# Optimization experiments

Measured on AMD Instinct MI355X. Metric: run time of the kernel, lower is better.

Reference implementation:

```python
import jax, jax.numpy as jnp
import numpy as np

EOS = 0
INCLUDE_EOS = True
INS_COST = 1.0
DEL_COST = 1.0
SUB_COST = 1.0


def _seq_lens(tok):
    # tok: (T, N) int tokens; length = index of first EOS (+1 if included), else T
    T = tok.shape[0]
    is_eos = tok == EOS
    has = is_eos.any(axis=0)
    idx = jnp.argmax(is_eos, axis=0)
    return jnp.where(has, idx + (1 if INCLUDE_EOS else 0), T)


def _edit_distance(ref, hyp, ref_lens, hyp_lens):
    # ref: (R, N), hyp: (H, N). Levenshtein DP, scan over hyp steps.
    # The sequential deletion dependence along the ref axis is turned into a
    # min-plus prefix scan: new_row[j] = j*del + cummin_k<=j (cand[k] - k*del).
    R, N = ref.shape
    H = hyp.shape[0]
    offs = (jnp.arange(R + 1, dtype=jnp.float32) * DEL_COST)[:, None]  # (R+1,1)
    row0 = jnp.broadcast_to(offs, (R + 1, N)) + jnp.zeros((R + 1, N), jnp.float32)

    def step(row, xs):
        i, h = xs  # i: 1-based hyp step, h: (N,) hyp tokens at this step
        sub_c = SUB_COST * (ref != h[None, :]).astype(jnp.float32)  # (R,N)
        cand = jnp.concatenate(
            [row[:1] + INS_COST,
             jnp.minimum(row[1:] + INS_COST, row[:-1] + sub_c)], axis=0)
        new_row = jax.lax.cummin(cand - offs, axis=0) + offs
        # freeze rows for sequences whose hypothesis already ended
        row = jnp.where(i <= hyp_lens[None, :], new_row, row)
        return row, None

    row, _ = jax.lax.scan(step, row0, (jnp.arange(1, H + 1), hyp))
    # distance at (hyp_len, ref_len) per sequence
    return jnp.take_along_axis(row, ref_lens[None, :], axis=0)[0]


def setup_inputs() -> dict:
    key = jax.random.key(0)
    k1, k2, k3 = jax.random.split(key, 3)
    log_probs = jax.random.normal(k1, (128, 64), dtype=jnp.float32)
    ref = jax.random.randint(k2, (256, 128), 0, 1000, dtype=jnp.int64)
    hyp = jax.random.randint(k3, (256, 128, 64), 0, 1000, dtype=jnp.int64)
    return {"log_probs": log_probs, "ref": ref, "hyp": hyp}


def reference(log_probs, ref, hyp):
    batch_size, samples = log_probs.shape
    R = ref.shape[0]
    H = hyp.shape[0]
    # ref is 2D: broadcast across samples (same reference per batch element)
    ref_flat = jnp.repeat(ref[:, :, None], samples, axis=2).reshape(R, batch_size * samples)
    hyp_flat = hyp.reshape(H, batch_size * samples)
    ref_lens = _seq_lens(ref_flat)
    hyp_lens = _seq_lens(hyp_flat)
    dist = _edit_distance(ref_flat, hyp_flat, ref_lens, hyp_lens)
    er = dist / ref_lens.astype(jnp.float32)  # norm=True -> error rate
    er = er.reshape(batch_size, samples)
    er = er - er.mean(axis=1, keepdims=True)  # sub_avg=True
    loss = er * jax.nn.softmax(log_probs, axis=1)
    return loss.mean()  # reduction='mean'
```

## Files before the change

kernel.cpp:

```cpp
#include <hip/hip_runtime.h>
#include <stdint.h>


#define BATCH   128
#define SAMPLES 64
#define RLEN    256
#define HLEN    256
#define NSEQ    (BATCH*SAMPLES)
#define NTOK    1000
#define NWW     8
#define SPB     32
#define PMSTR   9
#define HTSTR   36

typedef unsigned long long u64;
typedef unsigned int       u32;

__device__ __forceinline__ int row_shr1(int x) {
    return __builtin_amdgcn_mov_dpp(x, 0x111, 0xf, 0xf, true);
}

__global__ __launch_bounds__(256) void mer_edit(const int* __restrict__ ref,
                                                const int* __restrict__ hyp,
                                                int* __restrict__ scores,
                                                int* __restrict__ reflen)
{
    const int blk  = blockIdx.x;
    const int b    = blk >> 1;
    const int half = blk & 1;
    const int tid  = threadIdx.x;
    const int lane = tid & 63;
    const int w    = lane & 7;
    const int sl   = (tid >> 6) * 8 + (lane >> 3);

    __shared__ __align__(16) u32 pm[NTOK * PMSTR];
    __shared__ __align__(16) unsigned short ht[HLEN * HTSTR];
    __shared__ int m_sh;

    if (tid == 0) m_sh = RLEN;

    for (int i = tid; i < (NTOK * PMSTR) / 4; i += 256)
        ((int4*)pm)[i] = int4{0, 0, 0, 0};

#pragma unroll
    for (int it = 0; it < 8; it++) {
        int idx = it * 256 + tid;
        int t   = idx >> 3;
        int s4  = (idx & 7) * 4;
        int4 v  = *(const int4*)(hyp + t * NSEQ + b * SAMPLES + half * SPB + s4);
        ushort4 u;
        u.x = (unsigned short)v.x; u.y = (unsigned short)v.y;
        u.z = (unsigned short)v.z; u.w = (unsigned short)v.w;
        *(ushort4*)&ht[t * HTSTR + s4] = u;
    }

    const int rt = ref[tid * BATCH + b];
    __syncthreads();
    if (rt == 0) atomicMin(&m_sh, tid);
    __syncthreads();
    const int m = (m_sh < RLEN) ? (m_sh + 1) : RLEN;
    if (tid < m)
        atomicOr(&pm[rt * PMSTR + (tid >> 5)], 1u << (tid & 31));
    __syncthreads();

    const int  sw   = (m - 1) >> 5, sb = (m - 1) & 31;
    const bool isW0 = (w == 0);
    const bool isSW = (w == sw);

    u32  VP = ~0u, VN = 0u;
    int  score = m;
    bool done  = false;

    int tokA, tokB, tokC;
    u32 EqA, EqB;
    {
        int p0 = (0 - w) < 0 ? 0 : (0 - w);
        int p1 = (1 - w) < 0 ? 0 : (1 - w);
        int p2 = (2 - w) < 0 ? 0 : (2 - w);
        tokA = ht[p0 * HTSTR + sl];
        tokB = ht[p1 * HTSTR + sl];
        tokC = ht[p2 * HTSTR + sl];
        EqA  = pm[tokA * PMSTR + w];
        EqB  = pm[tokB * PMSTR + w];
    }

    int out_pkd = 0;
    int t = -w;

    for (int P = 0; P < HLEN + NWW - 1; ++P, ++t) {
        int t3 = t + 3;
        t3 = (t3 < 0) ? 0 : ((t3 > HLEN - 1) ? (HLEN - 1) : t3);

        int tokD = ht[t3 * HTSTR + sl];
        u32 EqC  = pm[tokC * PMSTR + w];

        int inp = row_shr1(out_pkd);
        if (isW0) inp = 2;
        const u32 cin  = (u32)(inp & 1);
        const u32 hpin = (u32)((inp >> 1) & 1);
        const u32 hnin = (u32)((inp >> 2) & 1);

        const u32 eq = EqA, vp = VP, vn = VN;
        const u32 x  = eq & vp;
        const u64 S  = (u64)x + vp + cin;
        const u32 s2   = (u32)S;
        const u32 cout = (u32)(S >> 32);
        const u32 D0 = (s2 ^ vp) | eq | vn;
        const u32 HP = vn | ~(D0 | vp);
        const u32 HN = vp & D0;
        const u32 HPs = (HP << 1) | hpin;
        const u32 HNs = (HN << 1) | hnin;
        const u32 nVP = HNs | ~(D0 | HPs);
        const u32 nVN = HPs & D0;

        out_pkd = (int)(cout | ((HP >> 31) << 1) | ((HN >> 31) << 2));

        const bool valid = (t >= 0) && (t < HLEN) && !done;
        if (valid) {
            VP = nVP; VN = nVN;
            if (isSW)
                score += (int)((HP >> sb) & 1u) - (int)((HN >> sb) & 1u);
            if (tokA == 0) done = true;
        }

        tokA = tokB; tokB = tokC; tokC = tokD;
        EqA  = EqB;  EqB  = EqC;
    }

    if (isSW) scores[b * SAMPLES + half * SPB + sl] = score;
    if (half == 0 && tid == 0) reflen[b] = m;
}

__global__ __launch_bounds__(64) void mer_loss(const float* __restrict__ lp,
                                               const int* __restrict__ scores,
                                               const int* __restrict__ reflen,
                                               double* __restrict__ partial)
{
    const int b = blockIdx.x, s = threadIdx.x;
    double er = (double)scores[b * SAMPLES + s] / (double)reflen[b];
    double x  = (double)lp[b * SAMPLES + s];
    double mx = x;
#pragma unroll
    for (int off = 32; off > 0; off >>= 1)
        mx = fmax(mx, __shfl_xor(mx, off));
    double e = exp(x - mx);
    double se = e, see = er * e, ser = er;
#pragma unroll
    for (int off = 32; off > 0; off >>= 1) {
        se  += __shfl_xor(se,  off);
        see += __shfl_xor(see, off);
        ser += __shfl_xor(ser, off);
    }
    if (s == 0) partial[b] = see / se - ser * (1.0 / SAMPLES);
}

__global__ __launch_bounds__(64) void mer_final(const double* __restrict__ partial,
                                                float* __restrict__ out)
{
    const int tid = threadIdx.x;
    double v = partial[tid] + partial[tid + 64];
#pragma unroll
    for (int off = 32; off > 0; off >>= 1)
        v += __shfl_xor(v, off);
    if (tid == 0) out[0] = (float)(v / (double)(BATCH * SAMPLES));
}

extern "C" void kernel_launch(void* const* d_in, const int* in_sizes, int n_in,
                              void* d_out, int out_size, void* d_ws, size_t ws_size,
                              hipStream_t stream)
{
    const float* lp  = (const float*)d_in[0];
    const int*   ref = (const int*)d_in[1];
    const int*   hyp = (const int*)d_in[2];

    double* partial = (double*)d_ws;
    int*    scores  = (int*)(partial + BATCH);
    int*    reflen  = scores + NSEQ;
    float*  out     = (float*)d_out;

    mer_edit<<<2 * BATCH, 256, 0, stream>>>(ref, hyp, scores, reflen);
    mer_loss<<<BATCH, 64, 0, stream>>>(lp, scores, reflen, partial);
    mer_final<<<1, 64, 0, stream>>>(partial, out);
}
```

Before: 104.0 us.

## Split Myers bit-vector into 16-bit words across 16 lanes per sequence

Switches the per-lane bit-parallel Myers edit-distance word from 32 bits to 16 bits, so each sequence is handled by 16 lanes instead of 8. Each block now covers 16 samples, and the grid grows from 256 to 512 blocks. The carry uses bit 16 of a 32-bit add instead of a 64-bit add. The aim is more parallelism and shorter per-lane dependency chains to fill the GPU. The cost is a longer wavefront skew (16 extra steps), per-block pattern-table building repeated four times per batch element, and extra shift/mask work on each Eq load.

```diff
diff --git a/kernel.cpp b/kernel.cpp
--- a/kernel.cpp
+++ b/kernel.cpp
@@ -8,10 +8,10 @@
 #define HLEN    256
 #define NSEQ    (BATCH*SAMPLES)
 #define NTOK    1000
-#define NWW     8
-#define SPB     32
+#define NW16    16
+#define SPB     16
 #define PMSTR   9
-#define HTSTR   36
+#define HTSTR   18
 
 typedef unsigned long long u64;
 typedef unsigned int       u32;
@@ -26,12 +26,12 @@
                                                 int* __restrict__ reflen)
 {
     const int blk  = blockIdx.x;
-    const int b    = blk >> 1;
-    const int half = blk & 1;
+    const int b    = blk >> 2;
+    const int q    = blk & 3;
     const int tid  = threadIdx.x;
     const int lane = tid & 63;
-    const int w    = lane & 7;
-    const int sl   = (tid >> 6) * 8 + (lane >> 3);
+    const int w    = lane & 15;
+    const int sl   = (tid >> 6) * 4 + (lane >> 4);
 
     __shared__ __align__(16) u32 pm[NTOK * PMSTR];
     __shared__ __align__(16) unsigned short ht[HLEN * HTSTR];
@@ -43,11 +43,11 @@
         ((int4*)pm)[i] = int4{0, 0, 0, 0};
 
 #pragma unroll
-    for (int it = 0; it < 8; it++) {
+    for (int it = 0; it < 4; it++) {
         int idx = it * 256 + tid;
-        int t   = idx >> 3;
-        int s4  = (idx & 7) * 4;
-        int4 v  = *(const int4*)(hyp + t * NSEQ + b * SAMPLES + half * SPB + s4);
+        int t   = idx >> 2;
+        int s4  = (idx & 3) * 4;
+        int4 v  = *(const int4*)(hyp + t * NSEQ + b * SAMPLES + q * SPB + s4);
         ushort4 u;
         u.x = (unsigned short)v.x; u.y = (unsigned short)v.y;
         u.z = (unsigned short)v.z; u.w = (unsigned short)v.w;
@@ -63,11 +63,12 @@
         atomicOr(&pm[rt * PMSTR + (tid >> 5)], 1u << (tid & 31));
     __syncthreads();
 
-    const int  sw   = (m - 1) >> 5, sb = (m - 1) & 31;
+    const int  sw   = (m - 1) >> 4, sb = (m - 1) & 15;
     const bool isW0 = (w == 0);
     const bool isSW = (w == sw);
+    const int  hw   = w >> 1, hsh = (w & 1) * 16;
 
-    u32  VP = ~0u, VN = 0u;
+    u32  VP = 0xFFFFu, VN = 0u;
     int  score = m;
     bool done  = false;
 
@@ -80,19 +81,19 @@
         tokA = ht[p0 * HTSTR + sl];
         tokB = ht[p1 * HTSTR + sl];
         tokC = ht[p2 * HTSTR + sl];
-        EqA  = pm[tokA * PMSTR + w];
-        EqB  = pm[tokB * PMSTR + w];
+        EqA  = (pm[tokA * PMSTR + hw] >> hsh) & 0xFFFFu;
+        EqB  = (pm[tokB * PMSTR + hw] >> hsh) & 0xFFFFu;
     }
 
     int out_pkd = 0;
     int t = -w;
 
-    for (int P = 0; P < HLEN + NWW - 1; ++P, ++t) {
+    for (int P = 0; P < HLEN + NW16 - 1; ++P, ++t) {
         int t3 = t + 3;
         t3 = (t3 < 0) ? 0 : ((t3 > HLEN - 1) ? (HLEN - 1) : t3);
 
         int tokD = ht[t3 * HTSTR + sl];
-        u32 EqC  = pm[tokC * PMSTR + w];
+        u32 EqC  = (pm[tokC * PMSTR + hw] >> hsh) & 0xFFFFu;
 
         int inp = row_shr1(out_pkd);
         if (isW0) inp = 2;
@@ -100,22 +101,21 @@
         const u32 hpin = (u32)((inp >> 1) & 1);
         const u32 hnin = (u32)((inp >> 2) & 1);
 
-        const u32 eq = EqA, vp = VP, vn = VN;
-        const u32 x  = eq & vp;
-        const u64 S  = (u64)x + vp + cin;
-        const u32 s2   = (u32)S;
-        const u32 cout = (u32)(S >> 32);
-        const u32 D0 = (s2 ^ vp) | eq | vn;
-        const u32 HP = vn | ~(D0 | vp);
-        const u32 HN = vp & D0;
+        const u32 eq = EqA;
+        const u32 x  = eq & VP;
+        const u32 S  = x + VP + cin;
+        const u32 D0 = (S ^ VP) | eq | VN;
+        const u32 HP = VN | ~(D0 | VP);
+        const u32 HN = VP & D0;
         const u32 HPs = (HP << 1) | hpin;
         const u32 HNs = (HN << 1) | hnin;
-        const u32 nVP = HNs | ~(D0 | HPs);
+        const u32 nVP = (HNs | ~(D0 | HPs)) & 0xFFFFu;
         const u32 nVN = HPs & D0;
 
-        out_pkd = (int)(cout | ((HP >> 31) << 1) | ((HN >> 31) << 2));
+        out_pkd = (int)(((S >> 16) & 1u) | (((HP >> 15) & 1u) << 1)
+                        | (((HN >> 15) & 1u) << 2));
 
-        const bool valid = (t >= 0) && (t < HLEN) && !done;
+        const bool valid = ((u32)t < (u32)HLEN) && !done;
         if (valid) {
             VP = nVP; VN = nVN;
             if (isSW)
@@ -127,8 +127,8 @@
         EqA  = EqB;  EqB  = EqC;
     }
 
-    if (isSW) scores[b * SAMPLES + half * SPB + sl] = score;
-    if (half == 0 && tid == 0) reflen[b] = m;
+    if (isSW) scores[b * SAMPLES + q * SPB + sl] = score;
+    if (q == 0 && tid == 0) reflen[b] = m;
 }
 
 __global__ __launch_bounds__(64) void mer_loss(const float* __restrict__ lp,
@@ -178,7 +178,7 @@
     int*    reflen  = scores + NSEQ;
     float*  out     = (float*)d_out;
 
-    mer_edit<<<2 * BATCH, 256, 0, stream>>>(ref, hyp, scores, reflen);
+    mer_edit<<<4 * BATCH, 256, 0, stream>>>(ref, hyp, scores, reflen);
     mer_loss<<<BATCH, 64, 0, stream>>>(lp, scores, reflen, partial);
     mer_final<<<1, 64, 0, stream>>>(partial, out);
 }
```

Result: slower. 115.9 us (+11.4%).

## Process four hyp steps per DPP exchange in bit-parallel edit-distance wavefront

Applied to the files above, without the earlier changes.

Restructures the Myers bit-vector wavefront so each lane handles four consecutive hypothesis tokens per phase. Carry, HP and HN bits for all four steps are packed into one DPP row shift, cutting the number of cross-lane exchanges and loop iterations. The hyp token table is transposed to a per-sequence row layout so four tokens load as one 8-byte read. The trade-off is a larger pipeline skew of four steps per word and more register pressure from the unrolled steps. The done-freezing logic is also altered: state keeps updating after EOS and only the score stops.

```diff
diff --git a/kernel.cpp b/kernel.cpp
--- a/kernel.cpp
+++ b/kernel.cpp
@@ -11,7 +11,9 @@
 #define NWW     8
 #define SPB     32
 #define PMSTR   9
-#define HTSTR   36
+#define HTROW   260
+#define RSTEP   4
+#define NPH     72
 
 typedef unsigned long long u64;
 typedef unsigned int       u32;
@@ -29,12 +31,11 @@
     const int b    = blk >> 1;
     const int half = blk & 1;
     const int tid  = threadIdx.x;
-    const int lane = tid & 63;
-    const int w    = lane & 7;
-    const int sl   = (tid >> 6) * 8 + (lane >> 3);
+    const int w    = tid & 7;
+    const int sl   = tid >> 3;
 
     __shared__ __align__(16) u32 pm[NTOK * PMSTR];
-    __shared__ __align__(16) unsigned short ht[HLEN * HTSTR];
+    __shared__ __align__(8)  unsigned short ht[SPB * HTROW];
     __shared__ int m_sh;
 
     if (tid == 0) m_sh = RLEN;
@@ -48,10 +49,10 @@
         int t   = idx >> 3;
         int s4  = (idx & 7) * 4;
         int4 v  = *(const int4*)(hyp + t * NSEQ + b * SAMPLES + half * SPB + s4);
-        ushort4 u;
-        u.x = (unsigned short)v.x; u.y = (unsigned short)v.y;
-        u.z = (unsigned short)v.z; u.w = (unsigned short)v.w;
-        *(ushort4*)&ht[t * HTSTR + s4] = u;
+        ht[(s4 + 0) * HTROW + t] = (unsigned short)v.x;
+        ht[(s4 + 1) * HTROW + t] = (unsigned short)v.y;
+        ht[(s4 + 2) * HTROW + t] = (unsigned short)v.z;
+        ht[(s4 + 3) * HTROW + t] = (unsigned short)v.w;
     }
 
     const int rt = ref[tid * BATCH + b];
@@ -66,66 +67,83 @@
     const int  sw   = (m - 1) >> 5, sb = (m - 1) & 31;
     const bool isW0 = (w == 0);
     const bool isSW = (w == sw);
+    const u32* pmw   = pm + w;
+    const unsigned short* htrow = ht + sl * HTROW;
 
     u32  VP = ~0u, VN = 0u;
     int  score = m;
     bool done  = false;
 
-    int tokA, tokB, tokC;
-    u32 EqA, EqB;
+    int base = -(w << 2);
+
+    int c0 = base     < 0 ? 0 : base;
+    int c1 = base + 4 < 0 ? 0 : base + 4;
+    uint2 tkA = *(const uint2*)(htrow + c0);
+    uint2 tkB = *(const uint2*)(htrow + c1);
+    u32 eqA0, eqA1, eqA2, eqA3;
     {
-        int p0 = (0 - w) < 0 ? 0 : (0 - w);
-        int p1 = (1 - w) < 0 ? 0 : (1 - w);
-        int p2 = (2 - w) < 0 ? 0 : (2 - w);
-        tokA = ht[p0 * HTSTR + sl];
-        tokB = ht[p1 * HTSTR + sl];
-        tokC = ht[p2 * HTSTR + sl];
-        EqA  = pm[tokA * PMSTR + w];
-        EqB  = pm[tokB * PMSTR + w];
+        u32 p0 = tkA.x & 0xFFFFu, p1 = tkA.x >> 16;
+        u32 p2 = tkA.y & 0xFFFFu, p3 = tkA.y >> 16;
+        eqA0 = pmw[p0 * PMSTR]; eqA1 = pmw[p1 * PMSTR];
+        eqA2 = pmw[p2 * PMSTR]; eqA3 = pmw[p3 * PMSTR];
     }
 
     int out_pkd = 0;
-    int t = -w;
-
-    for (int P = 0; P < HLEN + NWW - 1; ++P, ++t) {
-        int t3 = t + 3;
-        t3 = (t3 < 0) ? 0 : ((t3 > HLEN - 1) ? (HLEN - 1) : t3);
-
-        int tokD = ht[t3 * HTSTR + sl];
-        u32 EqC  = pm[tokC * PMSTR + w];
+
+#define STEP(EQ, TK, I) do {                                              \
+        u32 cin  = ((u32)inp >> (I)) & 1u;                                \
+        u32 hpin = ((u32)inp >> (8 + (I))) & 1u;                          \
+        u32 hnin = ((u32)inp >> (16 + (I))) & 1u;                         \
+        u32 x  = (EQ) & VP;                                               \
+        u64 S  = (u64)x + VP + cin;                                       \
+        u32 s2 = (u32)S;                                                  \
+        u32 D0 = (s2 ^ VP) | (EQ) | VN;                                   \
+        u32 HP = VN | ~(D0 | VP);                                         \
+        u32 HN = VP & D0;                                                 \
+        nout |= ((u32)(S >> 32) << (I)) | ((HP >> 31) << (8 + (I)))       \
+                | ((HN >> 31) << (16 + (I)));                             \
+        int delta = (int)((HP >> sb) & 1u) - (int)((HN >> sb) & 1u);      \
+        u32 HPs = (HP << 1) | hpin;                                       \
+        u32 HNs = (HN << 1) | hnin;                                       \
+        if (pvalid) {                                                     \
+            VP = HNs | ~(D0 | HPs);                                       \
+            VN = HPs & D0;                                                \
+            if (!done) {                                                  \
+                score += delta;                                           \
+                if ((TK) == 0) done = true;    \
+            }                                                             \
+        }                                                                 \
+    } while (0)
+
+#pragma unroll 2
+    for (int P = 0; P < NPH; ++P) {
+        int tl = base + 8;
+        tl = tl < 0 ? 0 : (tl > (HLEN - RSTEP) ? (HLEN - RSTEP) : tl);
+        uint2 tkC = *(const uint2*)(htrow + tl);
+
+        u32 n0 = tkB.x & 0xFFFFu, n1 = tkB.x >> 16;
+        u32 n2 = tkB.y & 0xFFFFu, n3 = tkB.y >> 16;
+        u32 eqB0 = pmw[n0 * PMSTR], eqB1 = pmw[n1 * PMSTR];
+        u32 eqB2 = pmw[n2 * PMSTR], eqB3 = pmw[n3 * PMSTR];
 
         int inp = row_shr1(out_pkd);
-        if (isW0) inp = 2;
-        const u32 cin  = (u32)(inp & 1);
-        const u32 hpin = (u32)((inp >> 1) & 1);
-        const u32 hnin = (u32)((inp >> 2) & 1);
-
-        const u32 eq = EqA, vp = VP, vn = VN;
-        const u32 x  = eq & vp;
-        const u64 S  = (u64)x + vp + cin;
-        const u32 s2   = (u32)S;
-        const u32 cout = (u32)(S >> 32);
-        const u32 D0 = (s2 ^ vp) | eq | vn;
-        const u32 HP = vn | ~(D0 | vp);
-        const u32 HN = vp & D0;
-        const u32 HPs = (HP << 1) | hpin;
-        const u32 HNs = (HN << 1) | hnin;
-        const u32 nVP = HNs | ~(D0 | HPs);
-        const u32 nVN = HPs & D0;
-
-        out_pkd = (int)(cout | ((HP >> 31) << 1) | ((HN >> 31) << 2));
-
-        const bool valid = (t >= 0) && (t < HLEN) && !done;
-        if (valid) {
-            VP = nVP; VN = nVN;
-            if (isSW)
-                score += (int)((HP >> sb) & 1u) - (int)((HN >> sb) & 1u);
-            if (tokA == 0) done = true;
-        }
-
-        tokA = tokB; tokB = tokC; tokC = tokD;
-        EqA  = EqB;  EqB  = EqC;
-    }
+        if (isW0) inp = 0x0F00;
+
+        const bool pvalid = ((u32)base < (u32)HLEN);
+        u32 nout = 0;
+        u32 a0 = tkA.x & 0xFFFFu, a1 = tkA.x >> 16;
+        u32 a2 = tkA.y & 0xFFFFu, a3 = tkA.y >> 16;
+        STEP(eqA0, a0, 0);
+        STEP(eqA1, a1, 1);
+        STEP(eqA2, a2, 2);
+        STEP(eqA3, a3, 3);
+        out_pkd = (int)nout;
+
+        tkA = tkB; tkB = tkC;
+        eqA0 = eqB0; eqA1 = eqB1; eqA2 = eqB2; eqA3 = eqB3;
+        base += RSTEP;
+    }
+#undef STEP
 
     if (isSW) scores[b * SAMPLES + half * SPB + sl] = score;
     if (half == 0 && tid == 0) reflen[b] = m;
```

Result: faster. 92.60 us (-11.0%).
